# Performance work log

Measured on AMD Instinct MI355X. Metric: run time of the kernel, lower is better.

## Reference

```python
import jax, jax.numpy as jnp
import numpy as np

B, L, E, H, D, DFF = 2, 2048, 1024, 16, 64, 4096
SCALE = D ** 0.5


def rmsnorm(x):
    # NOTE: original uses mean(x*x)**0.5 with no eps and no learned scale
    rms = jnp.sqrt(jnp.mean(x * x, axis=-1, keepdims=True))
    return x / rms


def alibi_matrix():
    i = jnp.arange(L)
    dists = -jnp.abs(i[None, :] - i[:, None]).astype(jnp.float32)  # [L, L]
    slopes = 2.0 ** (-jnp.linspace(1.0, 8.0, H))                   # [H]
    alibi = slopes[:, None, None] * dists                          # [H, L, L]
    causal = jnp.tril(jnp.ones((L, L), dtype=bool))
    return jnp.where(causal[None], alibi, -jnp.inf)[None]          # [1, H, L, L]


def setup_inputs() -> dict:
    key = jax.random.key(0)
    ks = jax.random.split(key, 16)
    s = 0.02
    return {
        "X": jax.random.normal(ks[0], (B, L, E), jnp.float32),
        "encoder_out": jax.random.normal(ks[1], (B, L, E), jnp.float32),
        # self-attention params
        "Wqkv": jax.random.normal(ks[2], (E, 3 * H * D), jnp.float32) * s,
        "bqkv": jnp.zeros((3 * H * D,), jnp.float32),
        "Wo_sa": jax.random.normal(ks[3], (H * D, E), jnp.float32) * s,
        "bo_sa": jnp.zeros((E,), jnp.float32),
        # cross-attention params (computed by torch module but its forward returns X, so unused)
        "Wq": jax.random.normal(ks[4], (E, H * D), jnp.float32) * s,
        "bq": jnp.zeros((H * D,), jnp.float32),
        "Wkv": jax.random.normal(ks[5], (E, 2 * H * D), jnp.float32) * s,
        "bkv": jnp.zeros((2 * H * D,), jnp.float32),
        "Wo_ca": jax.random.normal(ks[6], (H * D, E), jnp.float32) * s,
        "bo_ca": jnp.zeros((E,), jnp.float32),
        # GLU FFN params (bias=False)
        "Ww": jax.random.normal(ks[7], (E, DFF), jnp.float32) * s,
        "Wv": jax.random.normal(ks[8], (E, DFF), jnp.float32) * s,
        "Wout": jax.random.normal(ks[9], (DFF, E), jnp.float32) * s,
    }


def reference(X, encoder_out, Wqkv, bqkv, Wo_sa, bo_sa, Wq, bq, Wkv, bkv,
              Wo_ca, bo_ca, Ww, Wv, Wout):
    alibi = alibi_matrix()

    # ---- self-attention (pre-norm + residual) ----
    h = rmsnorm(X)
    qkv = (h @ Wqkv + bqkv).reshape(B, L, H, 3, D)
    Q, K, V = qkv[..., 0, :], qkv[..., 1, :], qkv[..., 2, :]      # [B, L, H, D]
    scores = jnp.einsum('blhd,bmhd->bhlm', Q, K) / SCALE + alibi  # [B, H, L, L]
    attn = jax.nn.softmax(scores, axis=-1)
    ctx = jnp.einsum('bhlm,bmhd->blhd', attn, V).reshape(B, L, H * D)
    X = X + ctx @ Wo_sa + bo_sa

    # ---- cross-attention stage ----
    # Faithful to source: CrossAttention.forward returns its input X (the
    # normalized tensor) rather than the attention output, so this block is
    # X + rmsnorm(X). Cross-attn params never affect the output.
    X = X + rmsnorm(X)

    # ---- GLU FFN (pre-norm + residual), exact (erf) GELU as in torch F.gelu ----
    h = rmsnorm(X)
    ff = jax.nn.gelu(h @ Ww, approximate=False) * (h @ Wv)
    X = X + ff @ Wout
    return X
```

## Files before the change

kernel.cpp:

```cpp
#include <hip/hip_runtime.h>

#define B_SZ 2
#define L_SEQ 2048
#define E_DIM 1024
#define NH 16
#define DH 64
#define DFF_DIM 4096
#define ROWS (B_SZ * L_SEQ)

typedef __attribute__((ext_vector_type(8))) short short8;
typedef __attribute__((ext_vector_type(4))) float f32x4;

__device__ __forceinline__ short f2bf(float f) {
  unsigned u = __builtin_bit_cast(unsigned, f);
  u = (u + 0x7FFFu + ((u >> 16) & 1u)) >> 16;
  return (short)u;
}
__device__ __forceinline__ float bf2f(short s) {
  unsigned u = ((unsigned)(unsigned short)s) << 16;
  return __builtin_bit_cast(float, u);
}

__device__ __forceinline__ void async_copy16(const void* g, void* l) {
  __builtin_amdgcn_global_load_lds(
      (const __attribute__((address_space(1))) void*)g,
      (__attribute__((address_space(3))) void*)l, 16, 0, 0);
}

__global__ __launch_bounds__(256) void transpose_f32_to_bf16(
    const float* __restrict__ W, short* __restrict__ Wt, int K, int N,
    int poff) {
  __shared__ float tile[32][33];
  int n0 = blockIdx.x * 32, k0 = blockIdx.y * 32;
  int tx = threadIdx.x & 31, ty = threadIdx.x >> 5;
#pragma unroll
  for (int i = 0; i < 4; i++)
    tile[ty + 8 * i][tx] = W[(size_t)(k0 + ty + 8 * i) * N + n0 + tx];
  __syncthreads();
#pragma unroll
  for (int i = 0; i < 4; i++) {
    int n = n0 + ty + 8 * i;
    int orow = (poff < 0) ? n : ((n >> 6) * 128 + (n & 63) + poff);
    Wt[(size_t)orow * K + k0 + tx] = f2bf(tile[tx][ty + 8 * i]);
  }
}

__device__ __forceinline__ float block_sum256(float v) {
  __shared__ float sbuf[4];
#pragma unroll
  for (int off = 32; off > 0; off >>= 1) v += __shfl_xor(v, off, 64);
  int lane = threadIdx.x & 63, w = threadIdx.x >> 6;
  if (lane == 0) sbuf[w] = v;
  __syncthreads();
  return sbuf[0] + sbuf[1] + sbuf[2] + sbuf[3];
}

__global__ __launch_bounds__(256) void rmsnorm_k(const float* __restrict__ X,
                                                 short* __restrict__ H) {
  size_t row = blockIdx.x;
  const float4* x4 = (const float4*)(X + row * E_DIM);
  float4 v = x4[threadIdx.x];
  float ss = v.x * v.x + v.y * v.y + v.z * v.z + v.w * v.w;
  ss = block_sum256(ss);
  float inv = rsqrtf(ss * (1.0f / E_DIM));
  short* h = H + row * E_DIM + (size_t)threadIdx.x * 4;
  h[0] = f2bf(v.x * inv);
  h[1] = f2bf(v.y * inv);
  h[2] = f2bf(v.z * inv);
  h[3] = f2bf(v.w * inv);
}

__global__ __launch_bounds__(256) void resid_rms_fused(
    const float* __restrict__ X, const float* __restrict__ P0,
    const float* __restrict__ P1, const float* __restrict__ bias,
    float* __restrict__ Xout, short* __restrict__ H) {
  size_t row = blockIdx.x;
  int t = threadIdx.x;
  float4 v = ((const float4*)(X + row * E_DIM))[t];
  float4 a = ((const float4*)(P0 + row * E_DIM))[t];
  float4 b = ((const float4*)(P1 + row * E_DIM))[t];
  float4 c = ((const float4*)bias)[t];
  v.x += a.x + b.x + c.x;
  v.y += a.y + b.y + c.y;
  v.z += a.z + b.z + c.z;
  v.w += a.w + b.w + c.w;
  float ss = v.x * v.x + v.y * v.y + v.z * v.z + v.w * v.w;
  ss = block_sum256(ss);
  float inv = rsqrtf(ss * (1.0f / E_DIM));
  float4 o;
  o.x = v.x * (1.0f + inv);
  o.y = v.y * (1.0f + inv);
  o.z = v.z * (1.0f + inv);
  o.w = v.w * (1.0f + inv);
  ((float4*)(Xout + row * E_DIM))[t] = o;
  short* h = H + row * E_DIM + (size_t)t * 4;
  h[0] = f2bf(v.x * inv);
  h[1] = f2bf(v.y * inv);
  h[2] = f2bf(v.z * inv);
  h[3] = f2bf(v.w * inv);
}

__global__ __launch_bounds__(256) void add2_k(const float* __restrict__ X2,
                                              const float* __restrict__ P0,
                                              const float* __restrict__ P1,
                                              float* __restrict__ out) {
  size_t i = (size_t)blockIdx.x * 256 + threadIdx.x;
  float4 v = ((const float4*)X2)[i];
  float4 a = ((const float4*)P0)[i];
  float4 b = ((const float4*)P1)[i];
  v.x += a.x + b.x;
  v.y += a.y + b.y;
  v.z += a.z + b.z;
  v.w += a.w + b.w;
  ((float4*)out)[i] = v;
}

__global__ __launch_bounds__(256, 2) void gemm_bt(
    const short* __restrict__ A, const short* __restrict__ Bt,
    const float* __restrict__ bias, const float* __restrict__ res,
    void* __restrict__ out, int M, int N, int K, int epi, int ksplit) {
  __shared__ short smem[128 * 32 * 2];
  short* As = smem;
  short* Bs = smem + 128 * 32;
  int t = threadIdx.x;
  int lane = t & 63;
  int quad = lane >> 4, l16 = lane & 15;
  int wave = t >> 6;
  int wr = wave >> 1, wc = wave & 1;
  int m0 = blockIdx.y * 128, n0 = blockIdx.x * 128;
  int klen = K / ksplit;
  int kstart = blockIdx.z * klen;

  f32x4 acc[4][4];
#pragma unroll
  for (int i = 0; i < 4; i++)
#pragma unroll
    for (int j = 0; j < 4; j++) acc[i][j] = (f32x4){0.f, 0.f, 0.f, 0.f};

  for (int k0 = kstart; k0 < kstart + klen; k0 += 32) {
    __syncthreads();
#pragma unroll
    for (int p = 0; p < 2; p++) {
      int s = p * 256 + t;
      int mm = s >> 2, kk = (s & 3) * 8;
      async_copy16(A + (size_t)(m0 + mm) * K + k0 + kk,
                   (char*)As + (size_t)s * 16);
      async_copy16(Bt + (size_t)(n0 + mm) * K + k0 + kk,
                   (char*)Bs + (size_t)s * 16);
    }
    __syncthreads();
    short8 af[4], bfv[4];
#pragma unroll
    for (int i = 0; i < 4; i++) {
      af[i] = *(const short8*)&As[(wr * 64 + i * 16 + l16) * 32 + quad * 8];
      bfv[i] = *(const short8*)&Bs[(wc * 64 + i * 16 + l16) * 32 + quad * 8];
    }
#pragma unroll
    for (int mi = 0; mi < 4; mi++)
#pragma unroll
      for (int ni = 0; ni < 4; ni++)
        acc[mi][ni] = __builtin_amdgcn_mfma_f32_16x16x32_bf16(
            af[mi], bfv[ni], acc[mi][ni], 0, 0, 0);
  }

  if (epi == 5) {
    __syncthreads();
    short* xbuf = smem;
    if (wc == 0) {
#pragma unroll
      for (int mi = 0; mi < 4; mi++)
#pragma unroll
        for (int ni = 0; ni < 4; ni++)
#pragma unroll
          for (int r = 0; r < 4; r++) {
            int rowl = wr * 64 + mi * 16 + quad * 4 + r;
            float v = acc[mi][ni][r];
            float g = 0.5f * v * (1.0f + erff(v * 0.70710678118654752f));
            xbuf[rowl * 64 + ni * 16 + l16] = f2bf(g);
          }
    }
    __syncthreads();
    if (wc == 1) {
      short* FF = (short*)out;
#pragma unroll
      for (int mi = 0; mi < 4; mi++)
#pragma unroll
        for (int ni = 0; ni < 4; ni++)
#pragma unroll
          for (int r = 0; r < 4; r++) {
            int rowl = wr * 64 + mi * 16 + quad * 4 + r;
            int coll = ni * 16 + l16;
            float w = bf2f(xbuf[rowl * 64 + coll]);
            FF[(size_t)(m0 + rowl) * DFF_DIM + blockIdx.x * 64 + coll] =
                f2bf(w * acc[mi][ni][r]);
          }
    }
    return;
  }

#pragma unroll
  for (int mi = 0; mi < 4; mi++) {
#pragma unroll
    for (int ni = 0; ni < 4; ni++) {
      int col = n0 + wc * 64 + ni * 16 + l16;
      float bv = bias ? bias[col] : 0.0f;
#pragma unroll
      for (int r = 0; r < 4; r++) {
        int row = m0 + wr * 64 + mi * 16 + quad * 4 + r;
        size_t idx = (size_t)row * N + col;
        float v = acc[mi][ni][r] + bv;
        if (epi == 0) {
          ((short*)out)[idx] = f2bf(v);
        } else if (epi == 3) {
          ((float*)out)[idx] = v + res[idx];
        } else {
          float* po = (float*)out + (size_t)blockIdx.z * ((size_t)M * N);
          po[idx] = v;
        }
      }
    }
  }
}

__global__ __launch_bounds__(256) void kv_prep(const short* __restrict__ qkv,
                                               short* __restrict__ Kh,
                                               short* __restrict__ VTh) {
  int lt = blockIdx.x, bh = blockIdx.y;
  int b = bh >> 4, h = bh & 15;
  __shared__ short vtile[64 * 72];
  int t = threadIdx.x;
  int r = t >> 3, c = (t & 7) * 8;
  const short* base =
      qkv + (size_t)(b * L_SEQ + lt * 64) * (3 * NH * DH) + h * (3 * DH);
#pragma unroll
  for (int p = 0; p < 2; p++) {
    int row = r + p * 32;
    short8 kv = *(const short8*)(base + (size_t)row * (3 * NH * DH) + DH + c);
    *(short8*)(Kh + ((size_t)bh * L_SEQ + lt * 64 + row) * DH + c) = kv;
    short8 vv =
        *(const short8*)(base + (size_t)row * (3 * NH * DH) + 2 * DH + c);
    *(short8*)&vtile[row * 72 + c] = vv;
  }
  __syncthreads();
#pragma unroll
  for (int p = 0; p < 2; p++) {
    int d = r + p * 32;
    short8 o;
#pragma unroll
    for (int u = 0; u < 8; u++) o[u] = vtile[(c + u) * 72 + d];
    *(short8*)(VTh + ((size_t)bh * DH + d) * L_SEQ + lt * 64 + c) = o;
  }
}

__global__ __launch_bounds__(256) void attn_k(const short* __restrict__ qkv,
                                              const short* __restrict__ Kh,
                                              const short* __restrict__ VTh,
                                              short* __restrict__ ctx) {
  int qt = (gridDim.x - 1) - blockIdx.x;
  int bh = blockIdx.y;
  int b = bh >> 4, h = bh & 15;
  int t = threadIdx.x;
  int wave = t >> 6, lane = t & 63;
  int quad = lane >> 4, l16 = lane & 15;

  __shared__ short kt[64 * 72];
  __shared__ short vt[64 * 72];
  __shared__ short pb[4 * 16 * 70];

  const float slope = exp2f(-(1.0f + (7.0f / 15.0f) * (float)h));
  const size_t rowstride = 3 * NH * DH;
  const short* qbase = qkv + (size_t)(b * L_SEQ) * rowstride + h * (3 * DH);
  int iw = qt * 64 + wave * 16;

  short8 qf[2];
  {
    const short* qp = qbase + (size_t)(iw + l16) * rowstride + quad * 8;
    qf[0] = *(const short8*)(qp);
    qf[1] = *(const short8*)(qp + 32);
  }

  f32x4 o[4];
#pragma unroll
  for (int i = 0; i < 4; i++) o[i] = (f32x4){0.f, 0.f, 0.f, 0.f};
  float rs[4] = {0.f, 0.f, 0.f, 0.f};
  float crow[4];
  int irow[4];
#pragma unroll
  for (int r = 0; r < 4; r++) {
    irow[r] = iw + quad * 4 + r;
    crow[r] = -slope * (float)irow[r] - 8.0f;
  }

  int sr = t >> 3, sc = (t & 7) * 8;
  const short* kg = Kh + (size_t)bh * L_SEQ * DH;
  const short* vg = VTh + (size_t)bh * DH * L_SEQ;
  short8 kreg[2], vreg[2];
  auto loadKV = [&](int j0) {
    kreg[0] = *(const short8*)(kg + (size_t)(j0 + sr) * DH + sc);
    kreg[1] = *(const short8*)(kg + (size_t)(j0 + sr + 32) * DH + sc);
    vreg[0] = *(const short8*)(vg + (size_t)sr * L_SEQ + j0 + sc);
    vreg[1] = *(const short8*)(vg + (size_t)(sr + 32) * L_SEQ + j0 + sc);
  };
  loadKV(0);

  short* pw = &pb[wave * 16 * 70];
  int ntile = qt + 1;
  for (int tix = 0; tix < ntile; ++tix) {
    int j0 = tix * 64;
    __syncthreads();
    *(short8*)&kt[sr * 72 + sc] = kreg[0];
    *(short8*)&kt[(sr + 32) * 72 + sc] = kreg[1];
    *(short8*)&vt[sr * 72 + sc] = vreg[0];
    *(short8*)&vt[(sr + 32) * 72 + sc] = vreg[1];
    __syncthreads();
    if (tix + 1 < ntile) loadKV(j0 + 64);

    f32x4 s[4];
#pragma unroll
    for (int nt = 0; nt < 4; nt++) {
      f32x4 a = (f32x4){0.f, 0.f, 0.f, 0.f};
#pragma unroll
      for (int ks = 0; ks < 2; ks++) {
        short8 bf =
            *(const short8*)&kt[(nt * 16 + l16) * 72 + ks * 32 + quad * 8];
        a = __builtin_amdgcn_mfma_f32_16x16x32_bf16(qf[ks], bf, a, 0, 0, 0);
      }
      s[nt] = a;
    }
    bool diag = (tix == ntile - 1);
#pragma unroll
    for (int nt = 0; nt < 4; nt++) {
      int j = j0 + nt * 16 + l16;
      float jb = slope * (float)j;
#pragma unroll
      for (int r = 0; r < 4; r++) {
        float v = __builtin_fmaf(s[nt][r], 0.125f, jb + crow[r]);
        if (diag && j > irow[r]) v = -1e30f;
        float p = __expf(v);
        rs[r] += p;
        pw[(quad * 4 + r) * 70 + nt * 16 + l16] = f2bf(p);
      }
    }
    short8 pf[2];
    pf[0] = *(const short8*)&pw[l16 * 70 + quad * 8];
    pf[1] = *(const short8*)&pw[l16 * 70 + 32 + quad * 8];
#pragma unroll
    for (int nt = 0; nt < 4; nt++) {
#pragma unroll
      for (int ks = 0; ks < 2; ks++) {
        short8 bv =
            *(const short8*)&vt[(nt * 16 + l16) * 72 + ks * 32 + quad * 8];
        o[nt] = __builtin_amdgcn_mfma_f32_16x16x32_bf16(pf[ks], bv, o[nt], 0,
                                                        0, 0);
      }
    }
  }
#pragma unroll
  for (int r = 0; r < 4; r++) {
#pragma unroll
    for (int off = 1; off < 16; off <<= 1) rs[r] += __shfl_xor(rs[r], off, 64);
    float inv = 1.0f / rs[r];
    short* dst = ctx + (size_t)(b * L_SEQ + irow[r]) * (NH * DH) + h * DH;
#pragma unroll
    for (int nt = 0; nt < 4; nt++) dst[nt * 16 + l16] = f2bf(o[nt][r] * inv);
  }
}

extern "C" void kernel_launch(void* const* d_in, const int* in_sizes, int n_in,
                              void* d_out, int out_size, void* d_ws,
                              size_t ws_size, hipStream_t stream) {
  const float* X = (const float*)d_in[0];
  const float* Wqkv = (const float*)d_in[2];
  const float* bqkv = (const float*)d_in[3];
  const float* Wo_sa = (const float*)d_in[4];
  const float* bo_sa = (const float*)d_in[5];
  const float* Ww = (const float*)d_in[12];
  const float* Wv = (const float*)d_in[13];
  const float* Wout = (const float*)d_in[14];

  char* ws = (char*)d_ws;
  auto take = [&](size_t bytes) {
    char* p = ws;
    ws += (bytes + 255) & ~(size_t)255;
    return p;
  };
  short* WqkvT = (short*)take((size_t)3 * NH * DH * E_DIM * 2);
  short* WoT = (short*)take((size_t)E_DIM * E_DIM * 2);
  short* Bcat = (short*)take((size_t)2 * DFF_DIM * E_DIM * 2);
  short* WoutT = (short*)take((size_t)E_DIM * DFF_DIM * 2);
  short* Hbuf = (short*)take((size_t)ROWS * E_DIM * 2);
  short* QKV = (short*)take((size_t)ROWS * 3 * NH * DH * 2);
  short* CTX = (short*)take((size_t)ROWS * NH * DH * 2);
  float* X1 = (float*)take((size_t)ROWS * E_DIM * 4);
  short* KVb = (short*)take((size_t)2 * B_SZ * NH * L_SEQ * DH * 2);
  short* FF = (short*)take((size_t)ROWS * DFF_DIM * 2);
  short* Kh = KVb;
  short* VTh = KVb + (size_t)B_SZ * NH * L_SEQ * DH;
  float* Pwo = (float*)FF;
  float* Pwout = (float*)QKV;
  (void)ws_size;
  (void)in_sizes;
  (void)n_in;
  (void)out_size;

  dim3 blk(256);
  transpose_f32_to_bf16<<<dim3(3072 / 32, 1024 / 32), blk, 0, stream>>>(
      Wqkv, WqkvT, 1024, 3072, -1);
  transpose_f32_to_bf16<<<dim3(1024 / 32, 1024 / 32), blk, 0, stream>>>(
      Wo_sa, WoT, 1024, 1024, -1);
  transpose_f32_to_bf16<<<dim3(4096 / 32, 1024 / 32), blk, 0, stream>>>(
      Ww, Bcat, 1024, 4096, 0);
  transpose_f32_to_bf16<<<dim3(4096 / 32, 1024 / 32), blk, 0, stream>>>(
      Wv, Bcat, 1024, 4096, 64);
  transpose_f32_to_bf16<<<dim3(1024 / 32, 4096 / 32), blk, 0, stream>>>(
      Wout, WoutT, 4096, 1024, -1);

  rmsnorm_k<<<ROWS, blk, 0, stream>>>(X, Hbuf);
  gemm_bt<<<dim3(3072 / 128, ROWS / 128), blk, 0, stream>>>(
      Hbuf, WqkvT, bqkv, nullptr, QKV, ROWS, 3072, 1024, 0, 1);
  kv_prep<<<dim3(L_SEQ / 64, B_SZ * NH), blk, 0, stream>>>(QKV, Kh, VTh);
  attn_k<<<dim3(L_SEQ / 64, B_SZ * NH), blk, 0, stream>>>(QKV, Kh, VTh, CTX);
  gemm_bt<<<dim3(1024 / 128, ROWS / 128, 2), blk, 0, stream>>>(
      CTX, WoT, nullptr, nullptr, Pwo, ROWS, 1024, 1024, 4, 2);
  resid_rms_fused<<<ROWS, blk, 0, stream>>>(
      X, Pwo, Pwo + (size_t)ROWS * E_DIM, bo_sa, X1, Hbuf);
  gemm_bt<<<dim3(2 * DFF_DIM / 128, ROWS / 128), blk, 0, stream>>>(
      Hbuf, Bcat, nullptr, nullptr, FF, ROWS, 2 * DFF_DIM, 1024, 5, 1);
  gemm_bt<<<dim3(1024 / 128, ROWS / 128, 2), blk, 0, stream>>>(
      FF, WoutT, nullptr, nullptr, Pwout, ROWS, 1024, 4096, 4, 2);
  add2_k<<<ROWS * E_DIM / (256 * 4), blk, 0, stream>>>(
      X1, Pwout, Pwout + (size_t)ROWS * E_DIM, (float*)d_out);
}
```

Baseline: 498.6 us.

## Merge weight transposes and rmsnorm into one launch; double GEMM K-step to 64

Combines the five weight transpose/convert kernels and the first rmsnorm into a single prep kernel that dispatches on block index, cutting five launches. The GEMM now loads 64 K-elements per barrier pair into two 32-wide LDS halves, halving the number of sync points per K loop at the cost of doubling LDS use per block. The GLU epilogue's staging buffer row stride is padded from 64 to 68 to reduce LDS bank conflicts, though the index at 68 stride for 128 rows may exceed the buffer's original assumptions (smem is now larger, so it fits).

Result: faster. 470.7 us (-5.6%).

```diff
diff --git a/kernel.cpp b/kernel.cpp
--- a/kernel.cpp
+++ b/kernel.cpp
@@ -27,24 +27,6 @@
       (__attribute__((address_space(3))) void*)l, 16, 0, 0);
 }
 
-__global__ __launch_bounds__(256) void transpose_f32_to_bf16(
-    const float* __restrict__ W, short* __restrict__ Wt, int K, int N,
-    int poff) {
-  __shared__ float tile[32][33];
-  int n0 = blockIdx.x * 32, k0 = blockIdx.y * 32;
-  int tx = threadIdx.x & 31, ty = threadIdx.x >> 5;
-#pragma unroll
-  for (int i = 0; i < 4; i++)
-    tile[ty + 8 * i][tx] = W[(size_t)(k0 + ty + 8 * i) * N + n0 + tx];
-  __syncthreads();
-#pragma unroll
-  for (int i = 0; i < 4; i++) {
-    int n = n0 + ty + 8 * i;
-    int orow = (poff < 0) ? n : ((n >> 6) * 128 + (n & 63) + poff);
-    Wt[(size_t)orow * K + k0 + tx] = f2bf(tile[tx][ty + 8 * i]);
-  }
-}
-
 __device__ __forceinline__ float block_sum256(float v) {
   __shared__ float sbuf[4];
 #pragma unroll
@@ -55,19 +37,63 @@
   return sbuf[0] + sbuf[1] + sbuf[2] + sbuf[3];
 }
 
-__global__ __launch_bounds__(256) void rmsnorm_k(const float* __restrict__ X,
-                                                 short* __restrict__ H) {
-  size_t row = blockIdx.x;
-  const float4* x4 = (const float4*)(X + row * E_DIM);
-  float4 v = x4[threadIdx.x];
-  float ss = v.x * v.x + v.y * v.y + v.z * v.z + v.w * v.w;
-  ss = block_sum256(ss);
-  float inv = rsqrtf(ss * (1.0f / E_DIM));
-  short* h = H + row * E_DIM + (size_t)threadIdx.x * 4;
-  h[0] = f2bf(v.x * inv);
-  h[1] = f2bf(v.y * inv);
-  h[2] = f2bf(v.z * inv);
-  h[3] = f2bf(v.w * inv);
+__global__ __launch_bounds__(256) void prep_all(
+    const float* __restrict__ Wqkv, const float* __restrict__ Wo,
+    const float* __restrict__ Ww, const float* __restrict__ Wv,
+    const float* __restrict__ Wout, const float* __restrict__ X,
+    short* __restrict__ WqkvT, short* __restrict__ WoT,
+    short* __restrict__ Bcat, short* __restrict__ WoutT,
+    short* __restrict__ H) {
+  __shared__ float tile[32][33];
+  int b = blockIdx.x;
+  if (b < 16384) {
+    const float* W;
+    short* Wt;
+    int K, N, poff, bx, by;
+    if (b < 3072) {
+      W = Wqkv; Wt = WqkvT; K = 1024; N = 3072; poff = -1;
+      bx = b % 96; by = b / 96;
+    } else if (b < 4096) {
+      int c = b - 3072;
+      W = Wo; Wt = WoT; K = 1024; N = 1024; poff = -1;
+      bx = c & 31; by = c >> 5;
+    } else if (b < 8192) {
+      int c = b - 4096;
+      W = Ww; Wt = Bcat; K = 1024; N = 4096; poff = 0;
+      bx = c & 127; by = c >> 7;
+    } else if (b < 12288) {
+      int c = b - 8192;
+      W = Wv; Wt = Bcat; K = 1024; N = 4096; poff = 64;
+      bx = c & 127; by = c >> 7;
+    } else {
+      int c = b - 12288;
+      W = Wout; Wt = WoutT; K = 4096; N = 1024; poff = -1;
+      bx = c & 31; by = c >> 5;
+    }
+    int n0 = bx * 32, k0 = by * 32;
+    int tx = threadIdx.x & 31, ty = threadIdx.x >> 5;
+#pragma unroll
+    for (int i = 0; i < 4; i++)
+      tile[ty + 8 * i][tx] = W[(size_t)(k0 + ty + 8 * i) * N + n0 + tx];
+    __syncthreads();
+#pragma unroll
+    for (int i = 0; i < 4; i++) {
+      int n = n0 + ty + 8 * i;
+      int orow = (poff < 0) ? n : ((n >> 6) * 128 + (n & 63) + poff);
+      Wt[(size_t)orow * K + k0 + tx] = f2bf(tile[tx][ty + 8 * i]);
+    }
+  } else {
+    size_t row = b - 16384;
+    float4 v = ((const float4*)(X + row * E_DIM))[threadIdx.x];
+    float ss = v.x * v.x + v.y * v.y + v.z * v.z + v.w * v.w;
+    ss = block_sum256(ss);
+    float inv = rsqrtf(ss * (1.0f / E_DIM));
+    short* h = H + row * E_DIM + (size_t)threadIdx.x * 4;
+    h[0] = f2bf(v.x * inv);
+    h[1] = f2bf(v.y * inv);
+    h[2] = f2bf(v.z * inv);
+    h[3] = f2bf(v.w * inv);
+  }
 }
 
 __global__ __launch_bounds__(256) void resid_rms_fused(
@@ -119,9 +145,11 @@
     const short* __restrict__ A, const short* __restrict__ Bt,
     const float* __restrict__ bias, const float* __restrict__ res,
     void* __restrict__ out, int M, int N, int K, int epi, int ksplit) {
-  __shared__ short smem[128 * 32 * 2];
-  short* As = smem;
-  short* Bs = smem + 128 * 32;
+  __shared__ short smem[128 * 32 * 4];
+  short* As0 = smem;
+  short* Bs0 = smem + 4096;
+  short* As1 = smem + 8192;
+  short* Bs1 = smem + 12288;
   int t = threadIdx.x;
   int lane = t & 63;
   int quad = lane >> 4, l16 = lane & 15;
@@ -137,30 +165,37 @@
 #pragma unroll
     for (int j = 0; j < 4; j++) acc[i][j] = (f32x4){0.f, 0.f, 0.f, 0.f};
 
-  for (int k0 = kstart; k0 < kstart + klen; k0 += 32) {
+  for (int k0 = kstart; k0 < kstart + klen; k0 += 64) {
     __syncthreads();
 #pragma unroll
     for (int p = 0; p < 2; p++) {
       int s = p * 256 + t;
       int mm = s >> 2, kk = (s & 3) * 8;
-      async_copy16(A + (size_t)(m0 + mm) * K + k0 + kk,
-                   (char*)As + (size_t)s * 16);
-      async_copy16(Bt + (size_t)(n0 + mm) * K + k0 + kk,
-                   (char*)Bs + (size_t)s * 16);
-    }
-    __syncthreads();
-    short8 af[4], bfv[4];
-#pragma unroll
-    for (int i = 0; i < 4; i++) {
-      af[i] = *(const short8*)&As[(wr * 64 + i * 16 + l16) * 32 + quad * 8];
-      bfv[i] = *(const short8*)&Bs[(wc * 64 + i * 16 + l16) * 32 + quad * 8];
-    }
-#pragma unroll
-    for (int mi = 0; mi < 4; mi++)
-#pragma unroll
-      for (int ni = 0; ni < 4; ni++)
-        acc[mi][ni] = __builtin_amdgcn_mfma_f32_16x16x32_bf16(
-            af[mi], bfv[ni], acc[mi][ni], 0, 0, 0);
+      const short* ag = A + (size_t)(m0 + mm) * K + k0 + kk;
+      const short* bg = Bt + (size_t)(n0 + mm) * K + k0 + kk;
+      async_copy16(ag, As0 + (size_t)s * 8);
+      async_copy16(bg, Bs0 + (size_t)s * 8);
+      async_copy16(ag + 32, As1 + (size_t)s * 8);
+      async_copy16(bg + 32, Bs1 + (size_t)s * 8);
+    }
+    __syncthreads();
+#pragma unroll
+    for (int half = 0; half < 2; half++) {
+      const short* As = half ? As1 : As0;
+      const short* Bs = half ? Bs1 : Bs0;
+      short8 af[4], bfv[4];
+#pragma unroll
+      for (int i = 0; i < 4; i++) {
+        af[i] = *(const short8*)&As[(wr * 64 + i * 16 + l16) * 32 + quad * 8];
+        bfv[i] = *(const short8*)&Bs[(wc * 64 + i * 16 + l16) * 32 + quad * 8];
+      }
+#pragma unroll
+      for (int mi = 0; mi < 4; mi++)
+#pragma unroll
+        for (int ni = 0; ni < 4; ni++)
+          acc[mi][ni] = __builtin_amdgcn_mfma_f32_16x16x32_bf16(
+              af[mi], bfv[ni], acc[mi][ni], 0, 0, 0);
+    }
   }
 
   if (epi == 5) {
@@ -176,7 +211,7 @@
             int rowl = wr * 64 + mi * 16 + quad * 4 + r;
             float v = acc[mi][ni][r];
             float g = 0.5f * v * (1.0f + erff(v * 0.70710678118654752f));
-            xbuf[rowl * 64 + ni * 16 + l16] = f2bf(g);
+            xbuf[rowl * 68 + ni * 16 + l16] = f2bf(g);
           }
     }
     __syncthreads();
@@ -190,7 +225,7 @@
           for (int r = 0; r < 4; r++) {
             int rowl = wr * 64 + mi * 16 + quad * 4 + r;
             int coll = ni * 16 + l16;
-            float w = bf2f(xbuf[rowl * 64 + coll]);
+            float w = bf2f(xbuf[rowl * 68 + coll]);
             FF[(size_t)(m0 + rowl) * DFF_DIM + blockIdx.x * 64 + coll] =
                 f2bf(w * acc[mi][ni][r]);
           }
@@ -404,18 +439,8 @@
   (void)out_size;
 
   dim3 blk(256);
-  transpose_f32_to_bf16<<<dim3(3072 / 32, 1024 / 32), blk, 0, stream>>>(
-      Wqkv, WqkvT, 1024, 3072, -1);
-  transpose_f32_to_bf16<<<dim3(1024 / 32, 1024 / 32), blk, 0, stream>>>(
-      Wo_sa, WoT, 1024, 1024, -1);
-  transpose_f32_to_bf16<<<dim3(4096 / 32, 1024 / 32), blk, 0, stream>>>(
-      Ww, Bcat, 1024, 4096, 0);
-  transpose_f32_to_bf16<<<dim3(4096 / 32, 1024 / 32), blk, 0, stream>>>(
-      Wv, Bcat, 1024, 4096, 64);
-  transpose_f32_to_bf16<<<dim3(1024 / 32, 4096 / 32), blk, 0, stream>>>(
-      Wout, WoutT, 4096, 1024, -1);
-
-  rmsnorm_k<<<ROWS, blk, 0, stream>>>(X, Hbuf);
+  prep_all<<<16384 + ROWS, blk, 0, stream>>>(Wqkv, Wo_sa, Ww, Wv, Wout, X,
+                                             WqkvT, WoT, Bcat, WoutT, Hbuf);
   gemm_bt<<<dim3(3072 / 128, ROWS / 128), blk, 0, stream>>>(
       Hbuf, WqkvT, bqkv, nullptr, QKV, ROWS, 3072, 1024, 0, 1);
   kv_prep<<<dim3(L_SEQ / 64, B_SZ * NH), blk, 0, stream>>>(QKV, Kh, VTh);
```
